# Optimization experiments

Measured on AMD Instinct MI355X. Metric: run time of the kernel, lower is better.

## Reference

```python
import jax, jax.numpy as jnp
import numpy as np

B, S, D, E = 8, 2048, 1024, 8
TOKENS = B * S
CAPACITY = TOKENS // E  # capacity_factor=1.0, top-1 gating (deepspeed default)


def _moe_layer(x_flat, Wg, We, be):
    """DeepSpeed-style top-1 MoE: gate -> capacity drop -> dispatch -> expert GEMM -> combine.
    x_flat: [T, D]; Wg: [D, E]; We: [E, D, D]; be: [E, D]."""
    gates = jax.nn.softmax(x_flat @ Wg, axis=-1)              # [T, E]
    idx = jnp.argmax(gates, axis=1)                            # [T] expert per token
    mask = jax.nn.one_hot(idx, E, dtype=jnp.int32)             # [T, E]
    loc = jnp.cumsum(mask, axis=0) - 1                         # position within expert
    loc_s = jnp.sum(loc * mask, axis=1)                        # [T]
    keep = loc_s < CAPACITY                                    # capacity drop
    gate_s = jnp.sum(gates * mask.astype(gates.dtype), axis=1) * keep.astype(gates.dtype)
    slot = jnp.clip(loc_s, 0, CAPACITY - 1)
    # dispatch: scatter kept tokens into [E, C, D] buffer (slots are unique for kept tokens)
    disp = jnp.zeros((E, CAPACITY, D), x_flat.dtype).at[idx, slot].add(
        x_flat * keep[:, None].astype(x_flat.dtype))
    # grouped expert GEMM
    eo = jnp.einsum('ecd,edf->ecf', disp, We) + be[:, None, :]  # [E, C, D]
    # combine: gather each token's expert output, scale by its gate value
    return eo[idx, slot] * gate_s[:, None]                      # [T, D]


def reference(x, y, W1, b1, Wg2, We2, be2, Wg3, We3, be3):
    h = jnp.einsum('bsd,df->bsf', x, W1) + b1                  # dense pre-layer
    hf = h.reshape(TOKENS, D)
    o = _moe_layer(hf, Wg2, We2, be2)
    o = _moe_layer(o, Wg3, We3, be3)
    h = h + o.reshape(B, S, D)                                 # residual add
    sent = h.mean(axis=1)                                      # [B, D]
    logp = jax.nn.log_softmax(sent, axis=-1)
    return -jnp.mean(logp[jnp.arange(B), y])                   # CrossEntropyLoss


def setup_inputs() -> dict:
    key = jax.random.key(0)
    ks = jax.random.split(key, 10)
    s = 0.02
    return {
        'x': jax.random.normal(ks[0], (B, S, D), jnp.float32),
        'y': jax.random.randint(ks[1], (B,), 0, D),
        'W1': jax.random.normal(ks[2], (D, D), jnp.float32) * s,
        'b1': jnp.zeros((D,), jnp.float32),
        'Wg2': jax.random.normal(ks[3], (D, E), jnp.float32) * s,
        'We2': jax.random.normal(ks[4], (E, D, D), jnp.float32) * s,
        'be2': jnp.zeros((E, D), jnp.float32),
        'Wg3': jax.random.normal(ks[5], (D, E), jnp.float32) * s,
        'We3': jax.random.normal(ks[6], (E, D, D), jnp.float32) * s,
        'be3': jnp.zeros((E, D), jnp.float32),
    }
```

## Files before the change

kernel.cpp:

```cpp
#include <hip/hip_runtime.h>
#include <hip/hip_bf16.h>
#include <math.h>


#define TOKS 16384
#define DIM 1024
#define NEXP 8
#define CAP 2048
#define BATCH 8
#define SEQ 2048

typedef __bf16 bf16_t;
typedef __bf16 bf16x8 __attribute__((ext_vector_type(8)));
typedef float fx4 __attribute__((ext_vector_type(4)));

__device__ __forceinline__ void gll16(const bf16_t* g, bf16_t* l) {
  __builtin_amdgcn_global_load_lds(
      (const __attribute__((address_space(1))) unsigned int*)g,
      (__attribute__((address_space(3))) unsigned int*)l, 16, 0, 0);
}

__global__ __launch_bounds__(256) void k_prep_w(
    const float* __restrict__ W1, const float* __restrict__ We2,
    const float* __restrict__ We3, bf16_t* __restrict__ Wt) {
  __shared__ float t[64][65];
  const int m = blockIdx.z;
  const float* src = (m == 0) ? W1
                     : (m <= 8) ? We2 + (size_t)(m - 1) * DIM * DIM
                                : We3 + (size_t)(m - 9) * DIM * DIM;
  bf16_t* dst = Wt + (size_t)m * DIM * DIM;
  const int n0 = blockIdx.x * 64, k0 = blockIdx.y * 64;
  const int tid = threadIdx.x;
  const int r = tid >> 4, c4 = (tid & 15) * 4;
#pragma unroll
  for (int i = 0; i < 4; i++) {
    float4 v = *(const float4*)&src[(size_t)(k0 + i * 16 + r) * DIM + n0 + c4];
    t[i * 16 + r][c4] = v.x;
    t[i * 16 + r][c4 + 1] = v.y;
    t[i * 16 + r][c4 + 2] = v.z;
    t[i * 16 + r][c4 + 3] = v.w;
  }
  __syncthreads();
#pragma unroll
  for (int i = 0; i < 4; i++) {
    int rn = i * 16 + r;
    union { bf16_t b[4]; uint2 u; } tmp;
#pragma unroll
    for (int j = 0; j < 4; j++) tmp.b[j] = (bf16_t)t[c4 + j][rn];
    *(uint2*)&dst[(size_t)(n0 + rn) * DIM + k0 + c4] = tmp.u;
  }
}

__global__ __launch_bounds__(256) void k_prep_wg(
    const float* __restrict__ Wg2, const float* __restrict__ Wg3,
    bf16_t* __restrict__ WgP) {
  const int which = blockIdx.x;
  const float* src = which ? Wg3 : Wg2;
  bf16_t* dst = WgP + which * (128 * 8 * 8);
  const int tid = threadIdx.x;
#pragma unroll
  for (int j = 0; j < 4; j++) {
    int d = tid * 4 + j;
    float4 a = *(const float4*)&src[d * 8];
    float4 b = *(const float4*)&src[d * 8 + 4];
    float v[8] = {a.x, a.y, a.z, a.w, b.x, b.y, b.z, b.w};
#pragma unroll
    for (int e = 0; e < 8; e++)
      dst[((d >> 3) * 8 + e) * 8 + (d & 7)] = (bf16_t)v[e];
  }
}

__global__ __launch_bounds__(256) void k_cvt_x(const float* __restrict__ x,
                                               bf16_t* __restrict__ xb) {
  size_t i = ((size_t)blockIdx.x * 256 + threadIdx.x) * 8;
  float4 a = *(const float4*)&x[i];
  float4 b = *(const float4*)&x[i + 4];
  union { bf16_t h[8]; uint4 u; } t;
  t.h[0] = (bf16_t)a.x; t.h[1] = (bf16_t)a.y; t.h[2] = (bf16_t)a.z; t.h[3] = (bf16_t)a.w;
  t.h[4] = (bf16_t)b.x; t.h[5] = (bf16_t)b.y; t.h[6] = (bf16_t)b.z; t.h[7] = (bf16_t)b.w;
  *(uint4*)&xb[i] = t.u;
}

__global__ __launch_bounds__(256) void k_gemm_dense(
    const bf16_t* __restrict__ A, const bf16_t* __restrict__ Bt,
    const float* __restrict__ bias, bf16_t* __restrict__ out) {
  __shared__ alignas(16) bf16_t As[128 * 64];
  __shared__ alignas(16) bf16_t Bs[128 * 64];
  const int tid = threadIdx.x;
  const int lane = tid & 63, wave = tid >> 6;
  const int quad = lane >> 4, l15 = lane & 15;
  const int wr = (wave >> 1) * 64, wc = (wave & 1) * 64;
  const int id = blockIdx.x;
  const int j_ = id >> 3;
  const int m0 = ((id & 7) * 16 + (j_ >> 3)) * 128;
  const int n0 = (j_ & 7) * 128;
  const int kc = (tid & 7) ^ ((tid >> 3) & 7);
  const int rbase = tid >> 3;

  const bf16_t* gA[4];
  const bf16_t* gB[4];
  bf16_t* lA[4];
  bf16_t* lB[4];
#pragma unroll
  for (int i = 0; i < 4; i++) {
    int r = rbase + 32 * i;
    gA[i] = A + (size_t)(m0 + r) * DIM + kc * 8;
    gB[i] = Bt + (size_t)(n0 + r) * DIM + kc * 8;
    lA[i] = &As[(wave * 64 + 256 * i) * 8];
    lB[i] = &Bs[(wave * 64 + 256 * i) * 8];
  }

  fx4 acc[4][4];
#pragma unroll
  for (int i = 0; i < 4; i++)
#pragma unroll
    for (int j = 0; j < 4; j++) acc[i][j] = (fx4)0.0f;

  for (int k0 = 0; k0 < DIM; k0 += 64) {
#pragma unroll
    for (int i = 0; i < 4; i++) gll16(gA[i] + k0, lA[i]);
#pragma unroll
    for (int i = 0; i < 4; i++) gll16(gB[i] + k0, lB[i]);
    __syncthreads();
#pragma unroll
    for (int s = 0; s < 2; s++) {
      const int pofs = ((s * 4 + quad) ^ (l15 & 7)) << 3;
      bf16x8 av[4], bv[4];
#pragma unroll
      for (int i = 0; i < 4; i++)
        av[i] = *(const bf16x8*)&As[(wr + i * 16 + l15) * 64 + pofs];
#pragma unroll
      for (int j = 0; j < 4; j++)
        bv[j] = *(const bf16x8*)&Bs[(wc + j * 16 + l15) * 64 + pofs];
#pragma unroll
      for (int i = 0; i < 4; i++)
#pragma unroll
        for (int j = 0; j < 4; j++)
          acc[i][j] = __builtin_amdgcn_mfma_f32_16x16x32_bf16(av[i], bv[j], acc[i][j], 0, 0, 0);
    }
    __syncthreads();
  }
#pragma unroll
  for (int j = 0; j < 4; j++) {
    int col = n0 + wc + j * 16 + l15;
    float bb = bias[col];
#pragma unroll
    for (int i = 0; i < 4; i++)
#pragma unroll
      for (int r = 0; r < 4; r++) {
        int m = m0 + wr + i * 16 + quad * 4 + r;
        out[(size_t)m * DIM + col] = (bf16_t)(acc[i][j][r] + bb);
      }
  }
}

__global__ __launch_bounds__(256) void k_gate_mm(
    const bf16_t* __restrict__ act, const bf16_t* __restrict__ WgP,
    int* __restrict__ idx, float* __restrict__ gate) {
  __shared__ alignas(16) bf16_t As[64 * 64];
  __shared__ alignas(16) bf16_t WgS[128 * 64];
  __shared__ float L[64][8];
  const int tid = threadIdx.x;
  const int lane = tid & 63, wave = tid >> 6;
  const int quad = lane >> 4, l15 = lane & 15;
  const int m0 = blockIdx.x * 64;
  const int kc = (tid & 7) ^ ((tid >> 3) & 7);
  const int rbase = tid >> 3;

#pragma unroll
  for (int j = 0; j < 4; j++)
    gll16(WgP + (j * 256 + wave * 64 + lane) * 8,
          &WgS[(j * 256 + wave * 64) * 8]);

  const bf16_t* gA[2];
  bf16_t* lA[2];
#pragma unroll
  for (int i = 0; i < 2; i++) {
    gA[i] = act + (size_t)(m0 + rbase + 32 * i) * DIM + kc * 8;
    lA[i] = &As[wave * 512 + i * 2048];
  }

  fx4 acc = (fx4)0.0f;
  for (int k0 = 0; k0 < DIM; k0 += 64) {
#pragma unroll
    for (int i = 0; i < 2; i++) gll16(gA[i] + k0, lA[i]);
    __syncthreads();
#pragma unroll
    for (int s = 0; s < 2; s++) {
      const int pofs = ((s * 4 + quad) ^ (l15 & 7)) << 3;
      bf16x8 av = *(const bf16x8*)&As[(wave * 16 + l15) * 64 + pofs];
      bf16x8 bv = *(const bf16x8*)&WgS[((k0 >> 3) + s * 4 + quad) * 64 + (l15 & 7) * 8];
      acc = __builtin_amdgcn_mfma_f32_16x16x32_bf16(av, bv, acc, 0, 0, 0);
    }
    __syncthreads();
  }
  if (l15 < 8) {
#pragma unroll
    for (int r = 0; r < 4; r++) L[wave * 16 + quad * 4 + r][l15] = acc[r];
  }
  __syncthreads();
  if (tid < 64) {
    float lg[8];
#pragma unroll
    for (int e = 0; e < 8; e++) lg[e] = L[tid][e];
    float best = lg[0];
    int bi = 0;
#pragma unroll
    for (int e = 1; e < 8; e++)
      if (lg[e] > best) { best = lg[e]; bi = e; }
    float s = 0.f;
#pragma unroll
    for (int e = 0; e < 8; e++) s += expf(lg[e] - best);
    idx[m0 + tid] = bi;
    gate[m0 + tid] = 1.0f / s;
  }
}

__global__ __launch_bounds__(1024) void k_route(
    const int* __restrict__ idx, int* __restrict__ tok, int* __restrict__ cnt,
    int* __restrict__ drop, int* __restrict__ ndrop) {
  const int e = blockIdx.x;
  const int tid = threadIdx.x, lane = tid & 63, wv = tid >> 6;
  __shared__ int wsum[16];
  const int4* p = (const int4*)(idx + tid * 16);
  int m[16];
  int c = 0;
#pragma unroll
  for (int j = 0; j < 4; j++) {
    int4 v = p[j];
    m[j * 4 + 0] = (v.x == e);
    m[j * 4 + 1] = (v.y == e);
    m[j * 4 + 2] = (v.z == e);
    m[j * 4 + 3] = (v.w == e);
    c += m[j * 4] + m[j * 4 + 1] + m[j * 4 + 2] + m[j * 4 + 3];
  }
  int sc = c;
#pragma unroll
  for (int off = 1; off < 64; off <<= 1) {
    int n = __shfl_up(sc, off);
    if (lane >= off) sc += n;
  }
  if (lane == 63) wsum[wv] = sc;
  __syncthreads();
  int wb = 0, tot = 0;
#pragma unroll
  for (int i = 0; i < 16; i++) {
    int s = wsum[i];
    tot += s;
    if (i < wv) wb += s;
  }
  int pos = wb + sc - c;
#pragma unroll
  for (int j = 0; j < 16; j++) {
    if (m[j]) {
      if (pos < CAP) {
        tok[e * CAP + pos] = tid * 16 + j;
      } else {
        int di = atomicAdd(ndrop, 1);
        drop[di] = tid * 16 + j;
      }
      pos++;
    }
  }
  if (tid == 0) cnt[e] = tot < CAP ? tot : CAP;
}

__global__ __launch_bounds__(128) void k_zero_rows(
    bf16_t* __restrict__ buf, const int* __restrict__ drop,
    const int* __restrict__ ndrop) {
  const int nd = *ndrop;
  const uint4 z = {0u, 0u, 0u, 0u};
  for (int j = blockIdx.x; j < nd; j += gridDim.x) {
    int t = drop[j];
    ((uint4*)(buf + (size_t)t * DIM))[threadIdx.x] = z;
  }
}

__global__ __launch_bounds__(256) void k_gemm_expert(
    const bf16_t* __restrict__ Ain, const bf16_t* __restrict__ Wt,
    const float* __restrict__ be, const int* __restrict__ tok,
    const int* __restrict__ cnt, const float* __restrict__ gate,
    const bf16_t* __restrict__ zp, bf16_t* __restrict__ outp) {
  const int id = blockIdx.x;
  const int e = id & 7;
  const int j_ = id >> 3;
  const int c0 = (j_ >> 3) * 128;
  const int n0 = (j_ & 7) * 128;
  const int count = cnt[e];
  if (c0 >= count) return;
  const bf16_t* Bt = Wt + (size_t)e * DIM * DIM;
  const float* bias = be + (size_t)e * DIM;
  const int* tk = tok + e * CAP;

  __shared__ alignas(16) bf16_t As[128 * 64];
  __shared__ alignas(16) bf16_t Bs[128 * 64];
  const int tid = threadIdx.x;
  const int lane = tid & 63, wave = tid >> 6;
  const int quad = lane >> 4, l15 = lane & 15;
  const int wr = (wave >> 1) * 64, wc = (wave & 1) * 64;
  const int kc = (tid & 7) ^ ((tid >> 3) & 7);
  const int rbase = tid >> 3;

  const bf16_t* gA[4];
  const bf16_t* gB[4];
  bf16_t* lA[4];
  bf16_t* lB[4];
#pragma unroll
  for (int i = 0; i < 4; i++) {
    int r = rbase + 32 * i;
    int ca = c0 + r;
    gA[i] = (ca < count) ? Ain + (size_t)tk[ca] * DIM + kc * 8 : zp;
    gB[i] = Bt + (size_t)(n0 + r) * DIM + kc * 8;
    lA[i] = &As[(wave * 64 + 256 * i) * 8];
    lB[i] = &Bs[(wave * 64 + 256 * i) * 8];
  }

  fx4 acc[4][4];
#pragma unroll
  for (int i = 0; i < 4; i++)
#pragma unroll
    for (int j = 0; j < 4; j++) acc[i][j] = (fx4)0.0f;

  for (int k0 = 0; k0 < DIM; k0 += 64) {
#pragma unroll
    for (int i = 0; i < 4; i++) gll16(gA[i] + k0, lA[i]);
#pragma unroll
    for (int i = 0; i < 4; i++) gll16(gB[i] + k0, lB[i]);
    __syncthreads();
#pragma unroll
    for (int s = 0; s < 2; s++) {
      const int pofs = ((s * 4 + quad) ^ (l15 & 7)) << 3;
      bf16x8 av[4], bv[4];
#pragma unroll
      for (int i = 0; i < 4; i++)
        av[i] = *(const bf16x8*)&As[(wr + i * 16 + l15) * 64 + pofs];
#pragma unroll
      for (int j = 0; j < 4; j++)
        bv[j] = *(const bf16x8*)&Bs[(wc + j * 16 + l15) * 64 + pofs];
#pragma unroll
      for (int i = 0; i < 4; i++)
#pragma unroll
        for (int j = 0; j < 4; j++)
          acc[i][j] = __builtin_amdgcn_mfma_f32_16x16x32_bf16(av[i], bv[j], acc[i][j], 0, 0, 0);
    }
    __syncthreads();
  }
#pragma unroll
  for (int i = 0; i < 4; i++)
#pragma unroll
    for (int r = 0; r < 4; r++) {
      int c = c0 + wr + i * 16 + quad * 4 + r;
      if (c < count) {
        int t = tk[c];
        float g = gate[t];
#pragma unroll
        for (int j = 0; j < 4; j++) {
          int col = n0 + wc + j * 16 + l15;
          outp[(size_t)t * DIM + col] = (bf16_t)((acc[i][j][r] + bias[col]) * g);
        }
      }
    }
}

__global__ __launch_bounds__(256) void k_reduce_sent(
    const bf16_t* __restrict__ h, const bf16_t* __restrict__ o2,
    float* __restrict__ sent) {
  const int tid = threadIdx.x;
  const int d8 = (tid & 127) * 8;
  const int sg = tid >> 7;
  const int b = blockIdx.y;
  const int s0 = blockIdx.x * 64 + sg * 32;
  float acc[8] = {0.f, 0.f, 0.f, 0.f, 0.f, 0.f, 0.f, 0.f};
  const size_t base = ((size_t)b * SEQ + s0) * DIM + d8;
  for (int i = 0; i < 32; i++) {
    union { bf16_t v[8]; uint4 u; } hh, oo;
    hh.u = *(const uint4*)&h[base + (size_t)i * DIM];
    oo.u = *(const uint4*)&o2[base + (size_t)i * DIM];
#pragma unroll
    for (int j = 0; j < 8; j++) acc[j] += (float)hh.v[j] + (float)oo.v[j];
  }
#pragma unroll
  for (int j = 0; j < 8; j++)
    atomicAdd(&sent[b * DIM + d8 + j], acc[j] * (1.0f / SEQ));
}

__global__ __launch_bounds__(256) void k_loss(
    const float* __restrict__ sent, const int* __restrict__ y,
    float* __restrict__ out) {
  const int b = blockIdx.x, tid = threadIdx.x;
  const float* sb = sent + b * DIM;
  __shared__ float red[256];
  float m = -1e30f;
  for (int d = tid; d < DIM; d += 256) m = fmaxf(m, sb[d]);
  red[tid] = m;
  __syncthreads();
  for (int s = 128; s; s >>= 1) {
    if (tid < s) red[tid] = fmaxf(red[tid], red[tid + s]);
    __syncthreads();
  }
  m = red[0];
  __syncthreads();
  float sum = 0.f;
  for (int d = tid; d < DIM; d += 256) sum += expf(sb[d] - m);
  red[tid] = sum;
  __syncthreads();
  for (int s = 128; s; s >>= 1) {
    if (tid < s) red[tid] += red[tid + s];
    __syncthreads();
  }
  if (tid == 0) atomicAdd(out, (m + logf(red[0]) - sb[y[b]]) * (1.0f / BATCH));
}

extern "C" void kernel_launch(void* const* d_in, const int* in_sizes, int n_in,
                              void* d_out, int out_size, void* d_ws, size_t ws_size,
                              hipStream_t stream) {
  (void)in_sizes; (void)n_in; (void)out_size; (void)ws_size;
  const float* x   = (const float*)d_in[0];
  const int*   y   = (const int*)d_in[1];
  const float* W1  = (const float*)d_in[2];
  const float* b1  = (const float*)d_in[3];
  const float* Wg2 = (const float*)d_in[4];
  const float* We2 = (const float*)d_in[5];
  const float* be2 = (const float*)d_in[6];
  const float* Wg3 = (const float*)d_in[7];
  const float* We3 = (const float*)d_in[8];
  const float* be3 = (const float*)d_in[9];

  char* p = (char*)d_ws;
  size_t off = 0;
  auto carve = [&](size_t bytes) -> char* {
    char* r = p + off;
    off += (bytes + 255) & ~(size_t)255;
    return r;
  };
  bf16_t* Wt   = (bf16_t*)carve((size_t)17 * DIM * DIM * 2);
  bf16_t* WgP  = (bf16_t*)carve(2 * 128 * 8 * 8 * 2);
  bf16_t* h    = (bf16_t*)carve((size_t)TOKS * DIM * 2);
  bf16_t* o1   = (bf16_t*)carve((size_t)TOKS * DIM * 2);
  bf16_t* o2   = (bf16_t*)carve((size_t)TOKS * DIM * 2);
  int*    idx  = (int*)carve(TOKS * 4);
  float*  gate = (float*)carve(TOKS * 4);
  int*    tok  = (int*)carve(NEXP * CAP * 4);
  int*    cnt  = (int*)carve(NEXP * 4);
  int*    drop2 = (int*)carve(TOKS * 4);
  int*    drop3 = (int*)carve(TOKS * 4);
  size_t zoff0 = off;
  float*  sent = (float*)carve(BATCH * DIM * 4);
  bf16_t* zp   = (bf16_t*)carve(4096);
  int*    nd2  = (int*)carve(256);
  int*    nd3  = (int*)carve(256);
  size_t zbytes = off - zoff0;
  bf16_t* xb   = o2;

  hipMemsetAsync(sent, 0, zbytes, stream);
  hipMemsetAsync(d_out, 0, 4, stream);

  k_prep_w<<<dim3(16, 16, 17), 256, 0, stream>>>(W1, We2, We3, Wt);
  k_prep_wg<<<2, 256, 0, stream>>>(Wg2, Wg3, WgP);
  k_cvt_x<<<TOKS * DIM / 8 / 256, 256, 0, stream>>>(x, xb);

  k_gemm_dense<<<(TOKS / 128) * (DIM / 128), 256, 0, stream>>>(xb, Wt, b1, h);

  k_gate_mm<<<TOKS / 64, 256, 0, stream>>>(h, WgP, idx, gate);
  k_route<<<NEXP, 1024, 0, stream>>>(idx, tok, cnt, drop2, nd2);
  k_zero_rows<<<256, 128, 0, stream>>>(o1, drop2, nd2);
  k_gemm_expert<<<NEXP * (CAP / 128) * (DIM / 128), 256, 0, stream>>>(
      h, Wt + (size_t)1 * DIM * DIM, be2, tok, cnt, gate, zp, o1);

  k_gate_mm<<<TOKS / 64, 256, 0, stream>>>(o1, WgP + 128 * 8 * 8, idx, gate);
  k_route<<<NEXP, 1024, 0, stream>>>(idx, tok, cnt, drop3, nd3);
  k_zero_rows<<<256, 128, 0, stream>>>(o2, drop3, nd3);
  k_gemm_expert<<<NEXP * (CAP / 128) * (DIM / 128), 256, 0, stream>>>(
      o1, Wt + (size_t)9 * DIM * DIM, be3, tok, cnt, gate, zp, o2);

  k_reduce_sent<<<dim3(SEQ / 64, BATCH), 256, 0, stream>>>(h, o2, sent);
  k_loss<<<BATCH, 256, 0, stream>>>(sent, y, (float*)d_out);
}
```

Baseline: 398.9 us.

## Fuse all stages into one persistent kernel with grid-wide barriers

Replaces the roughly fourteen separate kernel launches with a single persistent kernel of 1024 blocks that runs every stage in order, separated by a software grid barrier built on atomics. It also folds the sum over h into the epilogue of the dense GEMM through atomics, reworks routing to use per-thread bitmasks and to zero dropped rows inside the routing stage, and hoists the bias loads. The aim is to remove launch gaps and one full read of h. The cost is that ten grid-wide spin barriers will deadlock unless all 1024 blocks are resident at once, and many blocks sit idle in the small stages.

```diff
diff --git a/kernel.cpp b/kernel.cpp
--- a/kernel.cpp
+++ b/kernel.cpp
@@ -9,6 +9,7 @@
 #define CAP 2048
 #define BATCH 8
 #define SEQ 2048
+#define NBLK 1024
 
 typedef __bf16 bf16_t;
 typedef __bf16 bf16x8 __attribute__((ext_vector_type(8)));
@@ -20,87 +21,104 @@
       (__attribute__((address_space(3))) unsigned int*)l, 16, 0, 0);
 }
 
-__global__ __launch_bounds__(256) void k_prep_w(
-    const float* __restrict__ W1, const float* __restrict__ We2,
-    const float* __restrict__ We3, bf16_t* __restrict__ Wt) {
-  __shared__ float t[64][65];
-  const int m = blockIdx.z;
-  const float* src = (m == 0) ? W1
-                     : (m <= 8) ? We2 + (size_t)(m - 1) * DIM * DIM
-                                : We3 + (size_t)(m - 9) * DIM * DIM;
-  bf16_t* dst = Wt + (size_t)m * DIM * DIM;
-  const int n0 = blockIdx.x * 64, k0 = blockIdx.y * 64;
+__device__ __forceinline__ void gbar(int* bars) {
+  __syncthreads();
+  if (threadIdx.x == 0) {
+    __threadfence();
+    int gen = __hip_atomic_load(&bars[1], __ATOMIC_RELAXED, __HIP_MEMORY_SCOPE_AGENT);
+    int prev = __hip_atomic_fetch_add(&bars[0], 1, __ATOMIC_RELAXED, __HIP_MEMORY_SCOPE_AGENT);
+    if (prev == NBLK - 1) {
+      __hip_atomic_store(&bars[0], 0, __ATOMIC_RELAXED, __HIP_MEMORY_SCOPE_AGENT);
+      __threadfence();
+      __hip_atomic_store(&bars[1], gen + 1, __ATOMIC_RELAXED, __HIP_MEMORY_SCOPE_AGENT);
+    } else {
+      while (__hip_atomic_load(&bars[1], __ATOMIC_RELAXED, __HIP_MEMORY_SCOPE_AGENT) == gen)
+        __builtin_amdgcn_s_sleep(2);
+    }
+    __threadfence();
+  }
+  __syncthreads();
+}
+
+#define NJOB_W (17 * 256)
+#define NJOB_CVT (TOKS * DIM / 8 / 256)
+#define NJOBS (NJOB_W + 2 + NJOB_CVT)
+__device__ void st_prep(int id, const float* W1, const float* We2,
+                        const float* We3, const float* Wg2, const float* Wg3,
+                        const float* x, bf16_t* Wt, bf16_t* WgP, bf16_t* xb,
+                        char* smraw) {
   const int tid = threadIdx.x;
-  const int r = tid >> 4, c4 = (tid & 15) * 4;
-#pragma unroll
-  for (int i = 0; i < 4; i++) {
-    float4 v = *(const float4*)&src[(size_t)(k0 + i * 16 + r) * DIM + n0 + c4];
-    t[i * 16 + r][c4] = v.x;
-    t[i * 16 + r][c4 + 1] = v.y;
-    t[i * 16 + r][c4 + 2] = v.z;
-    t[i * 16 + r][c4 + 3] = v.w;
-  }
-  __syncthreads();
-#pragma unroll
-  for (int i = 0; i < 4; i++) {
-    int rn = i * 16 + r;
-    union { bf16_t b[4]; uint2 u; } tmp;
-#pragma unroll
-    for (int j = 0; j < 4; j++) tmp.b[j] = (bf16_t)t[c4 + j][rn];
-    *(uint2*)&dst[(size_t)(n0 + rn) * DIM + k0 + c4] = tmp.u;
-  }
-}
-
-__global__ __launch_bounds__(256) void k_prep_wg(
-    const float* __restrict__ Wg2, const float* __restrict__ Wg3,
-    bf16_t* __restrict__ WgP) {
-  const int which = blockIdx.x;
-  const float* src = which ? Wg3 : Wg2;
-  bf16_t* dst = WgP + which * (128 * 8 * 8);
-  const int tid = threadIdx.x;
-#pragma unroll
-  for (int j = 0; j < 4; j++) {
-    int d = tid * 4 + j;
-    float4 a = *(const float4*)&src[d * 8];
-    float4 b = *(const float4*)&src[d * 8 + 4];
-    float v[8] = {a.x, a.y, a.z, a.w, b.x, b.y, b.z, b.w};
-#pragma unroll
-    for (int e = 0; e < 8; e++)
-      dst[((d >> 3) * 8 + e) * 8 + (d & 7)] = (bf16_t)v[e];
-  }
-}
-
-__global__ __launch_bounds__(256) void k_cvt_x(const float* __restrict__ x,
-                                               bf16_t* __restrict__ xb) {
-  size_t i = ((size_t)blockIdx.x * 256 + threadIdx.x) * 8;
-  float4 a = *(const float4*)&x[i];
-  float4 b = *(const float4*)&x[i + 4];
-  union { bf16_t h[8]; uint4 u; } t;
-  t.h[0] = (bf16_t)a.x; t.h[1] = (bf16_t)a.y; t.h[2] = (bf16_t)a.z; t.h[3] = (bf16_t)a.w;
-  t.h[4] = (bf16_t)b.x; t.h[5] = (bf16_t)b.y; t.h[6] = (bf16_t)b.z; t.h[7] = (bf16_t)b.w;
-  *(uint4*)&xb[i] = t.u;
-}
-
-__global__ __launch_bounds__(256) void k_gemm_dense(
-    const bf16_t* __restrict__ A, const bf16_t* __restrict__ Bt,
-    const float* __restrict__ bias, bf16_t* __restrict__ out) {
-  __shared__ alignas(16) bf16_t As[128 * 64];
-  __shared__ alignas(16) bf16_t Bs[128 * 64];
+  for (int job = id; job < NJOBS; job += NBLK) {
+    if (job < NJOB_W) {
+      float(*t)[65] = (float(*)[65])smraw;
+      const int m = job >> 8, rem = job & 255;
+      const int n0 = (rem & 15) * 64, k0 = (rem >> 4) * 64;
+      const float* src = (m == 0) ? W1
+                         : (m <= 8) ? We2 + (size_t)(m - 1) * DIM * DIM
+                                    : We3 + (size_t)(m - 9) * DIM * DIM;
+      bf16_t* dst = Wt + (size_t)m * DIM * DIM;
+      const int r = tid >> 4, c4 = (tid & 15) * 4;
+#pragma unroll
+      for (int i = 0; i < 4; i++) {
+        float4 v = *(const float4*)&src[(size_t)(k0 + i * 16 + r) * DIM + n0 + c4];
+        t[i * 16 + r][c4] = v.x;
+        t[i * 16 + r][c4 + 1] = v.y;
+        t[i * 16 + r][c4 + 2] = v.z;
+        t[i * 16 + r][c4 + 3] = v.w;
+      }
+      __syncthreads();
+#pragma unroll
+      for (int i = 0; i < 4; i++) {
+        int rn = i * 16 + r;
+        union { bf16_t b[4]; uint2 u; } tmp;
+#pragma unroll
+        for (int j = 0; j < 4; j++) tmp.b[j] = (bf16_t)t[c4 + j][rn];
+        *(uint2*)&dst[(size_t)(n0 + rn) * DIM + k0 + c4] = tmp.u;
+      }
+      __syncthreads();
+    } else if (job < NJOB_W + 2) {
+      const int which = job - NJOB_W;
+      const float* src = which ? Wg3 : Wg2;
+      bf16_t* dst = WgP + which * (128 * 8 * 8);
+#pragma unroll
+      for (int j = 0; j < 4; j++) {
+        int d = tid * 4 + j;
+        float4 a = *(const float4*)&src[d * 8];
+        float4 b = *(const float4*)&src[d * 8 + 4];
+        float v[8] = {a.x, a.y, a.z, a.w, b.x, b.y, b.z, b.w};
+#pragma unroll
+        for (int e = 0; e < 8; e++)
+          dst[((d >> 3) * 8 + e) * 8 + (d & 7)] = (bf16_t)v[e];
+      }
+    } else {
+      const int cid = job - NJOB_W - 2;
+      size_t i = ((size_t)cid * 256 + tid) * 8;
+      float4 a = *(const float4*)&x[i];
+      float4 b = *(const float4*)&x[i + 4];
+      union { bf16_t h[8]; uint4 u; } t;
+      t.h[0] = (bf16_t)a.x; t.h[1] = (bf16_t)a.y; t.h[2] = (bf16_t)a.z; t.h[3] = (bf16_t)a.w;
+      t.h[4] = (bf16_t)b.x; t.h[5] = (bf16_t)b.y; t.h[6] = (bf16_t)b.z; t.h[7] = (bf16_t)b.w;
+      *(uint4*)&xb[i] = t.u;
+    }
+  }
+}
+
+__device__ void st_dense(int id, const bf16_t* A, const bf16_t* Bt,
+                         const float* bias, bf16_t* out, float* sent,
+                         char* smraw) {
+  bf16_t* As = (bf16_t*)smraw;
+  bf16_t* Bs = As + 128 * 64;
   const int tid = threadIdx.x;
   const int lane = tid & 63, wave = tid >> 6;
   const int quad = lane >> 4, l15 = lane & 15;
   const int wr = (wave >> 1) * 64, wc = (wave & 1) * 64;
-  const int id = blockIdx.x;
   const int j_ = id >> 3;
   const int m0 = ((id & 7) * 16 + (j_ >> 3)) * 128;
   const int n0 = (j_ & 7) * 128;
   const int kc = (tid & 7) ^ ((tid >> 3) & 7);
   const int rbase = tid >> 3;
 
-  const bf16_t* gA[4];
-  const bf16_t* gB[4];
-  bf16_t* lA[4];
-  bf16_t* lB[4];
+  const bf16_t* gA[4]; const bf16_t* gB[4]; bf16_t* lA[4]; bf16_t* lB[4];
 #pragma unroll
   for (int i = 0; i < 4; i++) {
     int r = rbase + 32 * i;
@@ -109,7 +127,6 @@
     lA[i] = &As[(wave * 64 + 256 * i) * 8];
     lB[i] = &Bs[(wave * 64 + 256 * i) * 8];
   }
-
   fx4 acc[4][4];
 #pragma unroll
   for (int i = 0; i < 4; i++)
@@ -140,46 +157,57 @@
     }
     __syncthreads();
   }
+  float bb[4], sj[4] = {0.f, 0.f, 0.f, 0.f};
+#pragma unroll
+  for (int j = 0; j < 4; j++) bb[j] = bias[n0 + wc + j * 16 + l15];
+#pragma unroll
+  for (int i = 0; i < 4; i++)
+#pragma unroll
+    for (int r = 0; r < 4; r++) {
+      int rowL = wr + i * 16 + quad * 4 + r;
+#pragma unroll
+      for (int j = 0; j < 4; j++) {
+        float v = acc[i][j][r] + bb[j];
+        sj[j] += v;
+        out[(size_t)(m0 + rowL) * DIM + n0 + wc + j * 16 + l15] = (bf16_t)v;
+      }
+    }
 #pragma unroll
   for (int j = 0; j < 4; j++) {
-    int col = n0 + wc + j * 16 + l15;
-    float bb = bias[col];
-#pragma unroll
-    for (int i = 0; i < 4; i++)
-#pragma unroll
-      for (int r = 0; r < 4; r++) {
-        int m = m0 + wr + i * 16 + quad * 4 + r;
-        out[(size_t)m * DIM + col] = (bf16_t)(acc[i][j][r] + bb);
-      }
-  }
-}
-
-__global__ __launch_bounds__(256) void k_gate_mm(
-    const bf16_t* __restrict__ act, const bf16_t* __restrict__ WgP,
-    int* __restrict__ idx, float* __restrict__ gate) {
-  __shared__ alignas(16) bf16_t As[64 * 64];
-  __shared__ alignas(16) bf16_t WgS[128 * 64];
-  __shared__ float L[64][8];
+    sj[j] += __shfl_xor(sj[j], 16);
+    sj[j] += __shfl_xor(sj[j], 32);
+  }
+  if (quad == 0) {
+#pragma unroll
+    for (int j = 0; j < 4; j++)
+      atomicAdd(&sent[(m0 >> 11) * DIM + n0 + wc + j * 16 + l15],
+                sj[j] * (1.0f / SEQ));
+  }
+}
+
+__device__ void st_gate(int id, const bf16_t* act, const bf16_t* WgPx,
+                        int* idx, float* gate, char* smraw) {
+  if (id >= 256) return;
+  bf16_t* As = (bf16_t*)smraw;
+  bf16_t* WgS = As + 64 * 64;
+  float* L = (float*)(WgS + 128 * 64);
   const int tid = threadIdx.x;
   const int lane = tid & 63, wave = tid >> 6;
   const int quad = lane >> 4, l15 = lane & 15;
-  const int m0 = blockIdx.x * 64;
+  const int m0 = id * 64;
   const int kc = (tid & 7) ^ ((tid >> 3) & 7);
   const int rbase = tid >> 3;
 
 #pragma unroll
   for (int j = 0; j < 4; j++)
-    gll16(WgP + (j * 256 + wave * 64 + lane) * 8,
-          &WgS[(j * 256 + wave * 64) * 8]);
-
-  const bf16_t* gA[2];
-  bf16_t* lA[2];
+    gll16(WgPx + (j * 256 + wave * 64 + lane) * 8, &WgS[(j * 256 + wave * 64) * 8]);
+
+  const bf16_t* gA[2]; bf16_t* lA[2];
 #pragma unroll
   for (int i = 0; i < 2; i++) {
     gA[i] = act + (size_t)(m0 + rbase + 32 * i) * DIM + kc * 8;
     lA[i] = &As[wave * 512 + i * 2048];
   }
-
   fx4 acc = (fx4)0.0f;
   for (int k0 = 0; k0 < DIM; k0 += 64) {
 #pragma unroll
@@ -196,13 +224,13 @@
   }
   if (l15 < 8) {
 #pragma unroll
-    for (int r = 0; r < 4; r++) L[wave * 16 + quad * 4 + r][l15] = acc[r];
+    for (int r = 0; r < 4; r++) L[(wave * 16 + quad * 4 + r) * 8 + l15] = acc[r];
   }
   __syncthreads();
   if (tid < 64) {
     float lg[8];
 #pragma unroll
-    for (int e = 0; e < 8; e++) lg[e] = L[tid][e];
+    for (int e = 0; e < 8; e++) lg[e] = L[tid * 8 + e];
     float best = lg[0];
     int bi = 0;
 #pragma unroll
@@ -216,24 +244,25 @@
   }
 }
 
-__global__ __launch_bounds__(1024) void k_route(
-    const int* __restrict__ idx, int* __restrict__ tok, int* __restrict__ cnt,
-    int* __restrict__ drop, int* __restrict__ ndrop) {
-  const int e = blockIdx.x;
+#define DLMAX 2048
+__device__ void st_route(int id, const int* idx, int* tok, int* cnt,
+                         bf16_t* obuf, char* smraw) {
+  if (id >= 8) return;
+  int* wsum = (int*)smraw;
+  int* dlist = wsum + 16;
+  const int e = id;
   const int tid = threadIdx.x, lane = tid & 63, wv = tid >> 6;
-  __shared__ int wsum[16];
-  const int4* p = (const int4*)(idx + tid * 16);
-  int m[16];
-  int c = 0;
-#pragma unroll
-  for (int j = 0; j < 4; j++) {
-    int4 v = p[j];
-    m[j * 4 + 0] = (v.x == e);
-    m[j * 4 + 1] = (v.y == e);
-    m[j * 4 + 2] = (v.z == e);
-    m[j * 4 + 3] = (v.w == e);
-    c += m[j * 4] + m[j * 4 + 1] + m[j * 4 + 2] + m[j * 4 + 3];
-  }
+  const int4* p4 = (const int4*)(idx + tid * 64);
+  unsigned long long mask = 0ull;
+#pragma unroll 4
+  for (int j = 0; j < 16; j++) {
+    int4 v = p4[j];
+    mask |= (unsigned long long)(v.x == e) << (4 * j);
+    mask |= (unsigned long long)(v.y == e) << (4 * j + 1);
+    mask |= (unsigned long long)(v.z == e) << (4 * j + 2);
+    mask |= (unsigned long long)(v.w == e) << (4 * j + 3);
+  }
+  int c = __popcll(mask);
   int sc = c;
 #pragma unroll
   for (int off = 1; off < 64; off <<= 1) {
@@ -244,56 +273,53 @@
   __syncthreads();
   int wb = 0, tot = 0;
 #pragma unroll
-  for (int i = 0; i < 16; i++) {
+  for (int i = 0; i < 4; i++) {
     int s = wsum[i];
     tot += s;
     if (i < wv) wb += s;
   }
   int pos = wb + sc - c;
-#pragma unroll
-  for (int j = 0; j < 16; j++) {
-    if (m[j]) {
+  const uint4 z = {0u, 0u, 0u, 0u};
+  for (int j = 0; j < 64; j++) {
+    if ((mask >> j) & 1ull) {
+      int t = tid * 64 + j;
       if (pos < CAP) {
-        tok[e * CAP + pos] = tid * 16 + j;
+        tok[e * CAP + pos] = t;
       } else {
-        int di = atomicAdd(ndrop, 1);
-        drop[di] = tid * 16 + j;
+        int di = pos - CAP;
+        if (di < DLMAX) dlist[di] = t;
+        else
+          for (int k = 0; k < 128; k++) *(uint4*)&obuf[(size_t)t * DIM + k * 8] = z;
       }
       pos++;
     }
   }
   if (tid == 0) cnt[e] = tot < CAP ? tot : CAP;
-}
-
-__global__ __launch_bounds__(128) void k_zero_rows(
-    bf16_t* __restrict__ buf, const int* __restrict__ drop,
-    const int* __restrict__ ndrop) {
-  const int nd = *ndrop;
-  const uint4 z = {0u, 0u, 0u, 0u};
-  for (int j = blockIdx.x; j < nd; j += gridDim.x) {
-    int t = drop[j];
-    ((uint4*)(buf + (size_t)t * DIM))[threadIdx.x] = z;
-  }
-}
-
-__global__ __launch_bounds__(256) void k_gemm_expert(
-    const bf16_t* __restrict__ Ain, const bf16_t* __restrict__ Wt,
-    const float* __restrict__ be, const int* __restrict__ tok,
-    const int* __restrict__ cnt, const float* __restrict__ gate,
-    const bf16_t* __restrict__ zp, bf16_t* __restrict__ outp) {
-  const int id = blockIdx.x;
+  __syncthreads();
+  int ndl = tot - CAP;
+  ndl = ndl < 0 ? 0 : (ndl > DLMAX ? DLMAX : ndl);
+  for (int d = tid >> 7; d < ndl; d += 2) {
+    int t = dlist[d];
+    *(uint4*)&obuf[(size_t)t * DIM + (tid & 127) * 8] = z;
+  }
+}
+
+__device__ void st_expert(int id, const bf16_t* Ain, const bf16_t* Wt8,
+                          const float* be, const int* tok, const int* cnt,
+                          const float* gate, const bf16_t* zp,
+                          bf16_t* outp, char* smraw) {
   const int e = id & 7;
   const int j_ = id >> 3;
   const int c0 = (j_ >> 3) * 128;
   const int n0 = (j_ & 7) * 128;
   const int count = cnt[e];
   if (c0 >= count) return;
-  const bf16_t* Bt = Wt + (size_t)e * DIM * DIM;
+  const bf16_t* Bt = Wt8 + (size_t)e * DIM * DIM;
   const float* bias = be + (size_t)e * DIM;
   const int* tk = tok + e * CAP;
 
-  __shared__ alignas(16) bf16_t As[128 * 64];
-  __shared__ alignas(16) bf16_t Bs[128 * 64];
+  bf16_t* As = (bf16_t*)smraw;
+  bf16_t* Bs = As + 128 * 64;
   const int tid = threadIdx.x;
   const int lane = tid & 63, wave = tid >> 6;
   const int quad = lane >> 4, l15 = lane & 15;
@@ -301,10 +327,7 @@
   const int kc = (tid & 7) ^ ((tid >> 3) & 7);
   const int rbase = tid >> 3;
 
-  const bf16_t* gA[4];
-  const bf16_t* gB[4];
-  bf16_t* lA[4];
-  bf16_t* lB[4];
+  const bf16_t* gA[4]; const bf16_t* gB[4]; bf16_t* lA[4]; bf16_t* lB[4];
 #pragma unroll
   for (int i = 0; i < 4; i++) {
     int r = rbase + 32 * i;
@@ -314,7 +337,6 @@
     lA[i] = &As[(wave * 64 + 256 * i) * 8];
     lB[i] = &Bs[(wave * 64 + 256 * i) * 8];
   }
-
   fx4 acc[4][4];
 #pragma unroll
   for (int i = 0; i < 4; i++)
@@ -345,6 +367,9 @@
     }
     __syncthreads();
   }
+  float bb[4];
+#pragma unroll
+  for (int j = 0; j < 4; j++) bb[j] = bias[n0 + wc + j * 16 + l15];
 #pragma unroll
   for (int i = 0; i < 4; i++)
 #pragma unroll
@@ -354,42 +379,39 @@
         int t = tk[c];
         float g = gate[t];
 #pragma unroll
-        for (int j = 0; j < 4; j++) {
-          int col = n0 + wc + j * 16 + l15;
-          outp[(size_t)t * DIM + col] = (bf16_t)((acc[i][j][r] + bias[col]) * g);
-        }
+        for (int j = 0; j < 4; j++)
+          outp[(size_t)t * DIM + n0 + wc + j * 16 + l15] =
+              (bf16_t)((acc[i][j][r] + bb[j]) * g);
       }
     }
 }
 
-__global__ __launch_bounds__(256) void k_reduce_sent(
-    const bf16_t* __restrict__ h, const bf16_t* __restrict__ o2,
-    float* __restrict__ sent) {
+__device__ void st_reduce(int id, const bf16_t* o2, float* sent) {
+  if (id >= 256) return;
   const int tid = threadIdx.x;
   const int d8 = (tid & 127) * 8;
   const int sg = tid >> 7;
-  const int b = blockIdx.y;
-  const int s0 = blockIdx.x * 64 + sg * 32;
+  const int b = id >> 5;
+  const int s0 = (id & 31) * 64 + sg * 32;
   float acc[8] = {0.f, 0.f, 0.f, 0.f, 0.f, 0.f, 0.f, 0.f};
   const size_t base = ((size_t)b * SEQ + s0) * DIM + d8;
   for (int i = 0; i < 32; i++) {
-    union { bf16_t v[8]; uint4 u; } hh, oo;
-    hh.u = *(const uint4*)&h[base + (size_t)i * DIM];
+    union { bf16_t v[8]; uint4 u; } oo;
     oo.u = *(const uint4*)&o2[base + (size_t)i * DIM];
 #pragma unroll
-    for (int j = 0; j < 8; j++) acc[j] += (float)hh.v[j] + (float)oo.v[j];
+    for (int j = 0; j < 8; j++) acc[j] += (float)oo.v[j];
   }
 #pragma unroll
   for (int j = 0; j < 8; j++)
     atomicAdd(&sent[b * DIM + d8 + j], acc[j] * (1.0f / SEQ));
 }
 
-__global__ __launch_bounds__(256) void k_loss(
-    const float* __restrict__ sent, const int* __restrict__ y,
-    float* __restrict__ out) {
-  const int b = blockIdx.x, tid = threadIdx.x;
+__device__ void st_loss(int id, const float* sent, const int* y, float* out,
+                        char* smraw) {
+  if (id >= 8) return;
+  float* red = (float*)smraw;
+  const int b = id, tid = threadIdx.x;
   const float* sb = sent + b * DIM;
-  __shared__ float red[256];
   float m = -1e30f;
   for (int d = tid; d < DIM; d += 256) m = fmaxf(m, sb[d]);
   red[tid] = m;
@@ -409,6 +431,36 @@
     __syncthreads();
   }
   if (tid == 0) atomicAdd(out, (m + logf(red[0]) - sb[y[b]]) * (1.0f / BATCH));
+}
+
+__global__ __launch_bounds__(256, 4) void k_mega(
+    const float* W1, const float* We2, const float* We3, const float* Wg2,
+    const float* Wg3, const float* x, const float* b1, const float* be2,
+    const float* be3, const int* y, bf16_t* Wt, bf16_t* WgP, bf16_t* xb,
+    bf16_t* h, bf16_t* o1, bf16_t* o2, int* idx, float* gate, int* tok,
+    int* cnt, float* sent, bf16_t* zp, int* bars, float* dout) {
+  __shared__ alignas(16) char smraw[32768];
+  const int id = blockIdx.x;
+
+  st_prep(id, W1, We2, We3, Wg2, Wg3, x, Wt, WgP, xb, smraw);
+  gbar(bars);
+  st_dense(id, xb, Wt, b1, h, sent, smraw);
+  gbar(bars);
+  st_gate(id, h, WgP, idx, gate, smraw);
+  gbar(bars);
+  st_route(id, idx, tok, cnt, o1, smraw);
+  gbar(bars);
+  st_expert(id, h, Wt + (size_t)1 * DIM * DIM, be2, tok, cnt, gate, zp, o1, smraw);
+  gbar(bars);
+  st_gate(id, o1, WgP + 128 * 8 * 8, idx, gate, smraw);
+  gbar(bars);
+  st_route(id, idx, tok, cnt, o2, smraw);
+  gbar(bars);
+  st_expert(id, o1, Wt + (size_t)9 * DIM * DIM, be3, tok, cnt, gate, zp, o2, smraw);
+  gbar(bars);
+  st_reduce(id, o2, sent);
+  gbar(bars);
+  st_loss(id, sent, y, dout, smraw);
 }
 
 extern "C" void kernel_launch(void* const* d_in, const int* in_sizes, int n_in,
@@ -442,37 +494,17 @@
   float*  gate = (float*)carve(TOKS * 4);
   int*    tok  = (int*)carve(NEXP * CAP * 4);
   int*    cnt  = (int*)carve(NEXP * 4);
-  int*    drop2 = (int*)carve(TOKS * 4);
-  int*    drop3 = (int*)carve(TOKS * 4);
   size_t zoff0 = off;
   float*  sent = (float*)carve(BATCH * DIM * 4);
   bf16_t* zp   = (bf16_t*)carve(4096);
-  int*    nd2  = (int*)carve(256);
-  int*    nd3  = (int*)carve(256);
+  int*    bars = (int*)carve(256);
   size_t zbytes = off - zoff0;
   bf16_t* xb   = o2;
 
   hipMemsetAsync(sent, 0, zbytes, stream);
   hipMemsetAsync(d_out, 0, 4, stream);
 
-  k_prep_w<<<dim3(16, 16, 17), 256, 0, stream>>>(W1, We2, We3, Wt);
-  k_prep_wg<<<2, 256, 0, stream>>>(Wg2, Wg3, WgP);
-  k_cvt_x<<<TOKS * DIM / 8 / 256, 256, 0, stream>>>(x, xb);
-
-  k_gemm_dense<<<(TOKS / 128) * (DIM / 128), 256, 0, stream>>>(xb, Wt, b1, h);
-
-  k_gate_mm<<<TOKS / 64, 256, 0, stream>>>(h, WgP, idx, gate);
-  k_route<<<NEXP, 1024, 0, stream>>>(idx, tok, cnt, drop2, nd2);
-  k_zero_rows<<<256, 128, 0, stream>>>(o1, drop2, nd2);
-  k_gemm_expert<<<NEXP * (CAP / 128) * (DIM / 128), 256, 0, stream>>>(
-      h, Wt + (size_t)1 * DIM * DIM, be2, tok, cnt, gate, zp, o1);
-
-  k_gate_mm<<<TOKS / 64, 256, 0, stream>>>(o1, WgP + 128 * 8 * 8, idx, gate);
-  k_route<<<NEXP, 1024, 0, stream>>>(idx, tok, cnt, drop3, nd3);
-  k_zero_rows<<<256, 128, 0, stream>>>(o2, drop3, nd3);
-  k_gemm_expert<<<NEXP * (CAP / 128) * (DIM / 128), 256, 0, stream>>>(
-      o1, Wt + (size_t)9 * DIM * DIM, be3, tok, cnt, gate, zp, o2);
-
-  k_reduce_sent<<<dim3(SEQ / 64, BATCH), 256, 0, stream>>>(h, o2, sent);
-  k_loss<<<BATCH, 256, 0, stream>>>(sent, y, (float*)d_out);
-}
+  k_mega<<<NBLK, 256, 0, stream>>>(
+      W1, We2, We3, Wg2, Wg3, x, b1, be2, be3, y, Wt, WgP, xb, h, o1, o2,
+      idx, gate, tok, cnt, sent, zp, bars, (float*)d_out);
+}
```

Result: slower. 1.483 ms (+271.8%).
